# Kernel tuning notes

Hardware: AMD Instinct MI355X
Metric: run time of the kernel (lower is better)

Reference implementation:

```python
import jax, jax.numpy as jnp
import numpy as np

DIM = 512; H = 8; TEMP_LEN = 16; TARGET_LEN = 22
NT = TEMP_LEN ** 2          # 256 temp tokens
NS = TARGET_LEN ** 2        # 484 target tokens
N = NT + NS                 # 740
HD = DIM // H
SCALE = HD ** -0.5
EPS = 1e-5
B = 16


def _bias_index(L):
    coords = np.stack(np.meshgrid(np.arange(L), np.arange(L), indexing='ij')).reshape(2, -1)
    rel = (coords[:, :, None] - coords[:, None, :]).transpose(1, 2, 0)  # [L^2, L^2, 2]
    rel[..., 0] += L - 1
    rel[..., 1] += L - 1
    rel[..., 0] *= 2 * L - 1
    return jnp.asarray(rel.sum(-1))  # [L^2, L^2] indices into (2L-1)^2 table

TEMP_IDX = _bias_index(TEMP_LEN)
TARGET_IDX = _bias_index(TARGET_LEN)


def setup_inputs() -> dict:
    key = jax.random.key(0)
    ctr = iter(range(100))
    def nrm(shape, s=1.0):
        return jax.random.normal(jax.random.fold_in(key, next(ctr)), shape, jnp.float32) * s
    def uni(shape):
        return jax.random.uniform(jax.random.fold_in(key, next(ctr)), shape, jnp.float32, 0.5, 1.5)
    d = {'x': nrm((B, N, DIM))}
    for nm in ('q', 'k', 'v'):
        d[f'conv_{nm}_w'] = nrm((DIM, 1, 3, 3), 0.2)   # depthwise 3x3, groups=DIM
        d[f'bn_{nm}_g'] = 1.0 + nrm((DIM,), 0.1)
        d[f'bn_{nm}_b'] = nrm((DIM,), 0.1)
        d[f'bn_{nm}_m'] = nrm((DIM,), 0.1)
        d[f'bn_{nm}_v'] = uni((DIM,))
    for nm in ('q', 'k', 'v', 'p'):
        d[f'w{nm}'] = nrm((DIM, DIM), DIM ** -0.5)
        d[f'b{nm}'] = nrm((DIM,), 0.01)
    d['rpb_target'] = nrm(((2 * TARGET_LEN - 1) ** 2, H), 0.0002)
    d['rpb_temp'] = nrm(((2 * TEMP_LEN - 1) ** 2, 1), 0.0002)
    d['tt_bias'] = nrm((H, 1, NT), 0.0002)       # temp_target_bias_table
    d['tg_tm_bias'] = nrm((H, NS, 1), 0.0002)    # target_temp_bias_table
    return d


def _dwconv_bn(z, w, g, b, m, v):
    # z: [B, C, Hh, Ww]; depthwise conv + BatchNorm2d (inference stats)
    y = jax.lax.conv_general_dilated(z, w, (1, 1), ((1, 1), (1, 1)),
                                     dimension_numbers=('NCHW', 'OIHW', 'NCHW'),
                                     feature_group_count=DIM)
    inv = (g * jax.lax.rsqrt(v + EPS))[None, :, None, None]
    return (y - m[None, :, None, None]) * inv + b[None, :, None, None]


def reference(x, conv_q_w, bn_q_g, bn_q_b, bn_q_m, bn_q_v,
              conv_k_w, bn_k_g, bn_k_b, bn_k_m, bn_k_v,
              conv_v_w, bn_v_g, bn_v_b, bn_v_m, bn_v_v,
              wq, bq, wk, bk, wv, bv, wp, bp,
              rpb_target, rpb_temp, tt_bias, tg_tm_bias):
    Bb = x.shape[0]
    to_img = lambda t, L: t.transpose(0, 2, 1).reshape(Bb, DIM, L, L)
    to_seq = lambda t: t.reshape(Bb, DIM, -1).transpose(0, 2, 1)
    ti = to_img(x[:, :NT], TEMP_LEN)
    tg = to_img(x[:, NT:], TARGET_LEN)

    def conv_branch(w, g, b, m, v):
        return jnp.concatenate([to_seq(_dwconv_bn(ti, w, g, b, m, v)),
                                to_seq(_dwconv_bn(tg, w, g, b, m, v))], axis=1)

    q = conv_branch(conv_q_w, bn_q_g, bn_q_b, bn_q_m, bn_q_v) @ wq + bq
    k = conv_branch(conv_k_w, bn_k_g, bn_k_b, bn_k_m, bn_k_v) @ wk + bk
    v = conv_branch(conv_v_w, bn_v_g, bn_v_b, bn_v_m, bn_v_v) @ wv + bv

    heads = lambda t: t.reshape(Bb, -1, H, HD).transpose(0, 2, 1, 3)
    qtm, ktm, vtm = heads(q[:, :NT]), heads(k[:, :NT]), heads(v[:, :NT])
    qta, kh, vh = heads(q[:, NT:]), heads(k), heads(v)

    # gathered relative-position bias tables
    target_bias = rpb_target[TARGET_IDX.reshape(-1)].reshape(NS, NS, H).transpose(2, 0, 1)  # [H,NS,NS]
    temp_bias = rpb_temp[TEMP_IDX.reshape(-1)].reshape(NT, NT, 1).transpose(2, 0, 1)        # [1,NT,NT]
    padding = tt_bias + tg_tm_bias                                                          # [H,NS,NT]
    rel = jnp.concatenate([padding, target_bias], axis=2)                                   # [H,NS,N]

    # target -> all attention
    attn = jax.nn.softmax(jnp.einsum('bhqd,bhkd->bhqk', qta, kh) * SCALE + rel, axis=-1)
    out_t = jnp.einsum('bhqk,bhkd->bhqd', attn, vh).transpose(0, 2, 1, 3).reshape(Bb, NS, DIM)

    # temp -> temp attention (bias broadcast over heads)
    attn2 = jax.nn.softmax(jnp.einsum('bhqd,bhkd->bhqk', qtm, ktm) * SCALE + temp_bias, axis=-1)
    out_m = jnp.einsum('bhqk,bhkd->bhqd', attn2, vtm).transpose(0, 2, 1, 3).reshape(Bb, NT, DIM)

    return jnp.concatenate([out_m, out_t], axis=1) @ wp + bp
```

## Files before the change

kernel.cpp:

```cpp
#include <hip/hip_runtime.h>
#include <hip/hip_bf16.h>

typedef unsigned short u16;
typedef unsigned int u32;
typedef __attribute__((ext_vector_type(8))) short short8;
typedef __attribute__((ext_vector_type(4))) float f32x4;

#define NTOK 740
#define NTMP 256
#define NTGT 484
#define DM   512
#define MH   8
#define MROWS 11840
#define KPAD 768
#define LOG2E 1.4426950408889634f

__device__ __forceinline__ float b2f(u16 u) {
    union { unsigned int i; float f; } x; x.i = ((unsigned int)u) << 16; return x.f;
}
__device__ __forceinline__ u16 f2b(float f) {
    union { float f; unsigned int i; } x; x.f = f;
    unsigned int r = x.i + 0x7FFFu + ((x.i >> 16) & 1u);
    return (u16)(r >> 16);
}
__device__ __forceinline__ u32 pk2(float a, float b) {
    union { __hip_bfloat162 h; u32 u; } p;
    p.h = __float22bfloat162_rn(float2{a, b});
    return p.u;
}
__device__ __forceinline__ float fexp2(float x) {
    return __builtin_amdgcn_exp2f(x);
}
struct alignas(8) us4 { u16 x, y, z, w; };

__device__ __forceinline__ void gload16(const void* g, void* l) {
    __builtin_amdgcn_global_load_lds(
        (const __attribute__((address_space(1))) void*)g,
        (__attribute__((address_space(3))) void*)l, 16, 0, 0);
}

__global__ __launch_bounds__(256) void prep_all(
    const float* __restrict__ w0, const float* __restrict__ w1,
    const float* __restrict__ w2, const float* __restrict__ w3, u16* __restrict__ wTbase,
    const float* __restrict__ cw0, const float* __restrict__ g0, const float* __restrict__ bb0,
    const float* __restrict__ m0, const float* __restrict__ v0,
    const float* __restrict__ cw1, const float* __restrict__ g1, const float* __restrict__ bb1,
    const float* __restrict__ m1, const float* __restrict__ v1,
    const float* __restrict__ cw2, const float* __restrict__ g2, const float* __restrict__ bb2,
    const float* __restrict__ m2, const float* __restrict__ v2,
    float* __restrict__ cwfb, float* __restrict__ shb,
    const float* __restrict__ rpb_t, const float* __restrict__ tt,
    const float* __restrict__ tg, u16* __restrict__ btab,
    const float* __restrict__ rpb_m, u16* __restrict__ mtab) {
    __shared__ float t[32][33];
    const int id = blockIdx.x, tid = threadIdx.x;
    if (id < 1024) {
        const int z = id >> 8, rem = id & 255;
        const int bx = rem & 15, by = rem >> 4;
        const float* W = z == 0 ? w0 : z == 1 ? w1 : z == 2 ? w2 : w3;
        u16* WT = wTbase + (size_t)z * 262144;
        const int tx = tid & 31, ty = tid >> 5;
        for (int i = ty; i < 32; i += 8)
            t[i][tx] = W[(size_t)(by * 32 + i) * 512 + bx * 32 + tx];
        __syncthreads();
        for (int i = ty; i < 32; i += 8)
            WT[(size_t)(bx * 32 + i) * 512 + by * 32 + tx] = f2b(t[tx][i]);
    } else if (id < 1051) {
        const int rem = id - 1024;
        const int tap = rem % 9, br = rem / 9;
        const float* cw = br == 0 ? cw0 : br == 1 ? cw1 : cw2;
        const float* g  = br == 0 ? g0  : br == 1 ? g1  : g2;
        const float* bb = br == 0 ? bb0 : br == 1 ? bb1 : bb2;
        const float* m  = br == 0 ? m0  : br == 1 ? m1  : m2;
        const float* v  = br == 0 ? v0  : br == 1 ? v1  : v2;
        for (int c = tid; c < DM; c += 256) {
            const float inv = g[c] * rsqrtf(v[c] + 1e-5f);
            cwfb[(br * 9 + tap) * DM + c] = cw[c * 9 + tap] * inv;
            if (tap == 0) shb[br * DM + c] = bb[c] - m[c] * inv;
        }
    } else if (id < 4923) {
        const int rem = id - 1051;
        const int h = rem / NTGT, q = rem % NTGT;
        const int qh = q / 22, qw = q % 22;
        const float tgv = tg[h * NTGT + q];
        for (int k = tid; k < KPAD; k += 256) {
            float val;
            if (k < NTMP) val = (tt[h * NTMP + k] + tgv) * LOG2E;
            else if (k < NTOK) {
                const int kj = k - NTMP, kh = kj / 22, kw = kj % 22;
                val = rpb_t[((qh - kh + 21) * 43 + (qw - kw + 21)) * MH + h] * LOG2E;
            } else val = -1e30f;
            btab[((size_t)(h * NTGT + q)) * KPAD + k] = f2b(val);
        }
    } else {
        const int q = id - 4923, k = tid;
        const int qh = q >> 4, qw = q & 15, kh = k >> 4, kw = k & 15;
        mtab[q * 256 + k] = f2b(rpb_m[(qh - kh + 15) * 31 + (qw - kw + 15)] * LOG2E);
    }
}

__global__ __launch_bounds__(256) void conv_bn3(
    const float* __restrict__ x,
    const float* __restrict__ cwfb, const float* __restrict__ shb,
    u16* __restrict__ o0, u16* __restrict__ o1, u16* __restrict__ o2) {
    const int bn = blockIdx.x * 2 + (threadIdx.x >> 7);
    const int c = (threadIdx.x & 127) * 4;
    const int b = bn / NTOK, n = bn % NTOK;
    const bool tmp = n < NTMP;
    const int L = tmp ? 16 : 22, base = tmp ? 0 : NTMP, p = n - base;
    const int ph = p / L, pw = p % L;
    float4 xv[9];
#pragma unroll
    for (int tap = 0; tap < 9; ++tap) {
        const int dh = tap / 3 - 1, dw = tap % 3 - 1;
        const int h2 = ph + dh, w2 = pw + dw;
        const bool ok = (h2 >= 0 && h2 < L && w2 >= 0 && w2 < L);
        xv[tap] = ok ? *(const float4*)(x + (size_t)(b * NTOK + base + h2 * L + w2) * DM + c)
                     : float4{0.f, 0.f, 0.f, 0.f};
    }
    const size_t o = (size_t)bn * DM + c;
    u16* out[3] = {o0, o1, o2};
#pragma unroll
    for (int br = 0; br < 3; ++br) {
        float4 acc = *(const float4*)(shb + br * DM + c);
#pragma unroll
        for (int tap = 0; tap < 9; ++tap) {
            const float4 wv = *(const float4*)(cwfb + (br * 9 + tap) * DM + c);
            acc.x = fmaf(wv.x, xv[tap].x, acc.x);
            acc.y = fmaf(wv.y, xv[tap].y, acc.y);
            acc.z = fmaf(wv.z, xv[tap].z, acc.z);
            acc.w = fmaf(wv.w, xv[tap].w, acc.w);
        }
        us4 r;
        r.x = f2b(acc.x); r.y = f2b(acc.y); r.z = f2b(acc.z); r.w = f2b(acc.w);
        *(us4*)(out[br] + o) = r;
    }
}

#define GEMM_BODY(A, BT)                                                             \
    const int tid = threadIdx.x;                                                     \
    const int lane = tid & 63, w = tid >> 6;                                         \
    const int lr = lane & 15, lg = lane >> 4;                                        \
    const int wm = (w >> 1) * 32, wn = (w & 1) * 64;                                 \
    const int srow4 = lane >> 2;                                                     \
    const int sc = (lane & 3) ^ (srow4 & 3);                                         \
    const u16* asrc  = A  + (size_t)(gm0 + w * 16 + srow4) * 512 + sc * 8;           \
    const u16* bsrc0 = BT + (size_t)(gn0 + w * 32 + srow4) * 512 + sc * 8;           \
    const u16* bsrc1 = BT + (size_t)(gn0 + w * 32 + 16 + srow4) * 512 + sc * 8;      \
    f32x4 acc[2][4] = {};                                                            \
    gload16(asrc, &As[0][w * 512]);                                                  \
    gload16(bsrc0, &Bs[0][w * 1024]);                                                \
    gload16(bsrc1, &Bs[0][w * 1024 + 512]);                                          \
    for (int kt = 0; kt < 16; ++kt) {                                                \
        const int cur = kt & 1;                                                      \
        if (kt < 15) {                                                               \
            gload16(asrc + (kt + 1) * 32, &As[cur ^ 1][w * 512]);                    \
            gload16(bsrc0 + (kt + 1) * 32, &Bs[cur ^ 1][w * 1024]);                  \
            gload16(bsrc1 + (kt + 1) * 32, &Bs[cur ^ 1][w * 1024 + 512]);            \
            asm volatile("s_waitcnt vmcnt(3)" ::: "memory");                         \
        } else {                                                                     \
            asm volatile("s_waitcnt vmcnt(0)" ::: "memory");                         \
        }                                                                            \
        __syncthreads();                                                             \
        short8 af[2], bfr[4];                                                        \
        _Pragma("unroll")                                                            \
        for (int i = 0; i < 2; ++i)                                                  \
            af[i] = *(const short8*)&As[cur][(wm + i * 16 + lr) * 32 + (lg ^ (lr & 3)) * 8]; \
        _Pragma("unroll")                                                            \
        for (int j = 0; j < 4; ++j)                                                  \
            bfr[j] = *(const short8*)&Bs[cur][(wn + j * 16 + lr) * 32 + (lg ^ (lr & 3)) * 8]; \
        _Pragma("unroll")                                                            \
        for (int i = 0; i < 2; ++i)                                                  \
            _Pragma("unroll")                                                        \
            for (int j = 0; j < 4; ++j)                                              \
                acc[i][j] = __builtin_amdgcn_mfma_f32_16x16x32_bf16(af[i], bfr[j], acc[i][j], 0, 0, 0); \
        __syncthreads();                                                             \
    }

__device__ __forceinline__ int xcd_remap(int hw, int n) {
    const int q8 = n >> 3, r8 = n & 7;
    const int xcd = hw & 7, i8 = hw >> 3;
    return (xcd < r8 ? xcd * (q8 + 1) : r8 * (q8 + 1) + (xcd - r8) * q8) + i8;
}

__global__ __launch_bounds__(256) void gemm_qkv(
    const u16* __restrict__ Aq, const u16* __restrict__ Ak, const u16* __restrict__ Av,
    const u16* __restrict__ wTb, const float* __restrict__ bq,
    const float* __restrict__ bk, const float* __restrict__ bv,
    u16* __restrict__ qout, u16* __restrict__ kout, u16* __restrict__ vbT, int zbase) {
    __shared__ u16 As[2][2048];
    __shared__ u16 Bs[2][4096];
    const int hw = blockIdx.x + 185 * (blockIdx.y + 4 * blockIdx.z);
    const int lid = xcd_remap(hw, 740 * gridDim.z);
    const int by = lid & 3;
    const int bx = (lid >> 2) % 185;
    const int z = lid / 740 + zbase;
    const int gm0 = bx * 64, gn0 = by * 128;
    const u16* A = z == 0 ? Aq : z == 1 ? Ak : Av;
    const u16* BT = wTb + (size_t)z * 262144;
    const float* bias = z == 0 ? bq : z == 1 ? bk : bv;
    GEMM_BODY(A, BT)
    u16* lin = z == 0 ? qout : kout;
#pragma unroll
    for (int i = 0; i < 2; ++i)
#pragma unroll
        for (int j = 0; j < 4; ++j) {
            const int gc = gn0 + wn + j * 16 + lr;
            const float bvl = bias[gc];
#pragma unroll
            for (int r = 0; r < 4; ++r) {
                const int gr = gm0 + wm + i * 16 + lg * 4 + r;
                const float val = acc[i][j][r] + bvl;
                if (z == 2) {
                    const int b2 = gr / NTOK, k = gr - b2 * NTOK;
                    const int hh = gc >> 6, d = gc & 63;
                    vbT[((size_t)(b2 * MH + hh) * 64 + d) * KPAD + k] = f2b(val);
                } else {
                    lin[(size_t)gr * 512 + gc] = f2b(val);
                }
            }
        }
}

__global__ __launch_bounds__(256) void gemm_out(const u16* __restrict__ Ain,
                                                const u16* __restrict__ BTin,
                                                const float* __restrict__ bias,
                                                float* __restrict__ C) {
    __shared__ u16 As[2][2048];
    __shared__ u16 Bs[2][4096];
    const int hw = blockIdx.x + 185 * blockIdx.y;
    const int lid = xcd_remap(hw, 740);
    const int by = lid & 3;
    const int bx = lid >> 2;
    const int gm0 = bx * 64, gn0 = by * 128;
    GEMM_BODY(Ain, BTin)
#pragma unroll
    for (int i = 0; i < 2; ++i)
#pragma unroll
        for (int j = 0; j < 4; ++j) {
            const int gc = gn0 + wn + j * 16 + lr;
            const float bvl = bias[gc];
#pragma unroll
            for (int r = 0; r < 4; ++r) {
                const int gr = gm0 + wm + i * 16 + lg * 4 + r;
                C[(size_t)gr * 512 + gc] = acc[i][j][r] + bvl;
            }
        }
}

__global__ __launch_bounds__(256) void attn_all(const u16* __restrict__ qb,
                                                const u16* __restrict__ kb,
                                                const u16* __restrict__ vbT,
                                                const u16* __restrict__ btab,
                                                const u16* __restrict__ mtab,
                                                u16* __restrict__ attb) {
    __shared__ u16 Ks[2][32][64];
    __shared__ u16 VTs[2][64][32];
    __shared__ u16 Pb[2][4][16][32];

    int wg = blockIdx.x + 6 * (blockIdx.y + 8 * blockIdx.z);
    wg = (wg & 7) * 96 + (wg >> 3);
    const int bx = wg % 6;
    const int hb = wg / 6;
    const int h = hb & 7, b = hb >> 3;

    const bool tgt = bx < 4;
    const int q0 = (tgt ? bx : bx - 4) * 128;
    const int NKr = tgt ? NTOK : NTMP;
    const int NCH = tgt ? 24 : 8;
    const int QTOT = tgt ? NTGT : NTMP;
    const int QOFF = tgt ? NTMP : 0;
    const int TK = tgt ? KPAD : 256;
    const int tid = threadIdx.x;
    const int w = tid >> 6, lane = tid & 63;
    const int lq = lane & 15, lg = lane >> 4;
    const int fq = (lq & 3) ^ ((lq >> 2) & 3);
    const size_t brow = (size_t)b * NTOK;
    const float SCL = 0.125f * LOG2E;

    int qA = q0 + w * 16 + lq;       if (qA > QTOT - 1) qA = QTOT - 1;
    int qB = q0 + 64 + w * 16 + lq;  if (qB > QTOT - 1) qB = QTOT - 1;
    const u16* tbase = tgt ? (btab + (size_t)h * NTGT * KPAD) : mtab;
    const u16* trowA = tbase + (size_t)qA * TK;
    const u16* trowB = tbase + (size_t)qB * TK;

    short8 qfA[2], qfB[2];
#pragma unroll
    for (int dc = 0; dc < 2; ++dc) {
        qfA[dc] = *(const short8*)(qb + (brow + QOFF + qA) * DM + h * 64 + dc * 32 + lg * 8);
        qfB[dc] = *(const short8*)(qb + (brow + QOFF + qB) * DM + h * 64 + dc * 32 + lg * 8);
    }

    const int krow = tid >> 3, ksc = tid & 7;
    const int vrow = tid >> 2, vsc = tid & 3;
    const int fv = (vrow & 3) ^ ((vrow >> 2) & 3);
    const size_t vbase = (size_t)(b * MH + h) * 64 * KPAD;
    const u16* kptr2 = kb + brow * DM + h * 64 + (ksc ^ (krow & 7)) * 8;
    const u16* vptr2 = vbT + vbase + (size_t)vrow * KPAD + (vsc ^ fv) * 8;
    const int NKm1 = NKr - 1;

    float mrunA = -1e30f, lrunA = 0.f, mrunB = -1e30f, lrunB = 0.f;
    f32x4 oTA[4] = {}, oTB[4] = {};

    {
        const int keyc = krow < NKm1 ? krow : NKm1;
        gload16(kptr2 + (size_t)keyc * DM, &Ks[0][w * 8][0]);
        gload16(vptr2, &VTs[0][w * 16][0]);
    }
    us4 bcA0 = *(const us4*)(trowA + lg * 4);
    us4 bcA1 = *(const us4*)(trowA + 16 + lg * 4);
    us4 bcB0 = *(const us4*)(trowB + lg * 4);
    us4 bcB1 = *(const us4*)(trowB + 16 + lg * 4);
    asm volatile("s_waitcnt vmcnt(0)" ::: "memory");
    __syncthreads();

    for (int kc = 0; kc < NCH; ++kc) {
        const int cur = kc & 1, nxt = cur ^ 1;
        const bool more = (kc + 1 < NCH);
        us4 bnA0 = {0,0,0,0}, bnA1 = {0,0,0,0}, bnB0 = {0,0,0,0}, bnB1 = {0,0,0,0};
        if (more) {
            const int key = (kc + 1) * 32 + krow;
            const int keyc = key < NKm1 ? key : NKm1;
            gload16(kptr2 + (size_t)keyc * DM, &Ks[nxt][w * 8][0]);
            gload16(vptr2 + (kc + 1) * 32, &VTs[nxt][w * 16][0]);
            bnA0 = *(const us4*)(trowA + (kc + 1) * 32 + lg * 4);
            bnA1 = *(const us4*)(trowA + (kc + 1) * 32 + 16 + lg * 4);
            bnB0 = *(const us4*)(trowB + (kc + 1) * 32 + lg * 4);
            bnB1 = *(const us4*)(trowB + (kc + 1) * 32 + 16 + lg * 4);
        }

        f32x4 sA0 = {}, sA1 = {}, sB0 = {}, sB1 = {};
        __builtin_amdgcn_s_setprio(1);
#pragma unroll
        for (int dc = 0; dc < 2; ++dc) {
            short8 a0 = *(const short8*)&Ks[cur][lq][((dc * 4 + lg) ^ (lq & 7)) * 8];
            short8 a1 = *(const short8*)&Ks[cur][16 + lq][((dc * 4 + lg) ^ (lq & 7)) * 8];
            sA0 = __builtin_amdgcn_mfma_f32_16x16x32_bf16(a0, qfA[dc], sA0, 0, 0, 0);
            sB0 = __builtin_amdgcn_mfma_f32_16x16x32_bf16(a0, qfB[dc], sB0, 0, 0, 0);
            sA1 = __builtin_amdgcn_mfma_f32_16x16x32_bf16(a1, qfA[dc], sA1, 0, 0, 0);
            sB1 = __builtin_amdgcn_mfma_f32_16x16x32_bf16(a1, qfB[dc], sB1, 0, 0, 0);
        }
        __builtin_amdgcn_s_setprio(0);

        {
            float sv[8];
            sv[0] = fmaf(sA0[0], SCL, b2f(bcA0.x)); sv[1] = fmaf(sA0[1], SCL, b2f(bcA0.y));
            sv[2] = fmaf(sA0[2], SCL, b2f(bcA0.z)); sv[3] = fmaf(sA0[3], SCL, b2f(bcA0.w));
            sv[4] = fmaf(sA1[0], SCL, b2f(bcA1.x)); sv[5] = fmaf(sA1[1], SCL, b2f(bcA1.y));
            sv[6] = fmaf(sA1[2], SCL, b2f(bcA1.z)); sv[7] = fmaf(sA1[3], SCL, b2f(bcA1.w));
            float cm = sv[0];
#pragma unroll
            for (int i = 1; i < 8; ++i) cm = fmaxf(cm, sv[i]);
            cm = fmaxf(cm, __shfl_xor(cm, 16));
            cm = fmaxf(cm, __shfl_xor(cm, 32));
            if (!__all(cm <= mrunA)) {
                const float mnew = fmaxf(mrunA, cm);
                const float alpha = fexp2(mrunA - mnew);
#pragma unroll
                for (int t = 0; t < 4; ++t)
#pragma unroll
                    for (int r = 0; r < 4; ++r) oTA[t][r] *= alpha;
                lrunA *= alpha;
                mrunA = mnew;
            }
            float pv[8], psum = 0.f;
#pragma unroll
            for (int i = 0; i < 8; ++i) { pv[i] = fexp2(sv[i] - mrunA); psum += pv[i]; }
            const int c0 = (((lg >> 1) ^ fq) & 3) * 8 + (lg & 1) * 4;
            const int c1 = (((2 + (lg >> 1)) ^ fq) & 3) * 8 + (lg & 1) * 4;
            *(uint2*)&Pb[0][w][lq][c0] = uint2{pk2(pv[0], pv[1]), pk2(pv[2], pv[3])};
            *(uint2*)&Pb[0][w][lq][c1] = uint2{pk2(pv[4], pv[5]), pk2(pv[6], pv[7])};
            psum += __shfl_xor(psum, 16);
            psum += __shfl_xor(psum, 32);
            lrunA += psum;
        }
        {
            float sv[8];
            sv[0] = fmaf(sB0[0], SCL, b2f(bcB0.x)); sv[1] = fmaf(sB0[1], SCL, b2f(bcB0.y));
            sv[2] = fmaf(sB0[2], SCL, b2f(bcB0.z)); sv[3] = fmaf(sB0[3], SCL, b2f(bcB0.w));
            sv[4] = fmaf(sB1[0], SCL, b2f(bcB1.x)); sv[5] = fmaf(sB1[1], SCL, b2f(bcB1.y));
            sv[6] = fmaf(sB1[2], SCL, b2f(bcB1.z)); sv[7] = fmaf(sB1[3], SCL, b2f(bcB1.w));
            float cm = sv[0];
#pragma unroll
            for (int i = 1; i < 8; ++i) cm = fmaxf(cm, sv[i]);
            cm = fmaxf(cm, __shfl_xor(cm, 16));
            cm = fmaxf(cm, __shfl_xor(cm, 32));
            if (!__all(cm <= mrunB)) {
                const float mnew = fmaxf(mrunB, cm);
                const float alpha = fexp2(mrunB - mnew);
#pragma unroll
                for (int t = 0; t < 4; ++t)
#pragma unroll
                    for (int r = 0; r < 4; ++r) oTB[t][r] *= alpha;
                lrunB *= alpha;
                mrunB = mnew;
            }
            float pv[8], psum = 0.f;
#pragma unroll
            for (int i = 0; i < 8; ++i) { pv[i] = fexp2(sv[i] - mrunB); psum += pv[i]; }
            const int c0 = (((lg >> 1) ^ fq) & 3) * 8 + (lg & 1) * 4;
            const int c1 = (((2 + (lg >> 1)) ^ fq) & 3) * 8 + (lg & 1) * 4;
            *(uint2*)&Pb[1][w][lq][c0] = uint2{pk2(pv[0], pv[1]), pk2(pv[2], pv[3])};
            *(uint2*)&Pb[1][w][lq][c1] = uint2{pk2(pv[4], pv[5]), pk2(pv[6], pv[7])};
            psum += __shfl_xor(psum, 16);
            psum += __shfl_xor(psum, 32);
            lrunB += psum;
        }

        asm volatile("s_waitcnt lgkmcnt(0)" ::: "memory");

        short8 pfA = *(const short8*)&Pb[0][w][lq][((lg ^ fq) & 3) * 8];
        short8 pfB = *(const short8*)&Pb[1][w][lq][((lg ^ fq) & 3) * 8];
        __builtin_amdgcn_s_setprio(1);
#pragma unroll
        for (int t = 0; t < 4; ++t) {
            short8 vf = *(const short8*)&VTs[cur][t * 16 + lq][((lg ^ fq) & 3) * 8];
            oTA[t] = __builtin_amdgcn_mfma_f32_16x16x32_bf16(vf, pfA, oTA[t], 0, 0, 0);
            oTB[t] = __builtin_amdgcn_mfma_f32_16x16x32_bf16(vf, pfB, oTB[t], 0, 0, 0);
        }
        __builtin_amdgcn_s_setprio(0);

        bcA0 = bnA0; bcA1 = bnA1; bcB0 = bnB0; bcB1 = bnB1;
        asm volatile("s_waitcnt vmcnt(0)" ::: "memory");
        __syncthreads();
    }

    {
        const float linv = 1.f / lrunA;
        const int qrow = q0 + w * 16 + lq;
        if (qrow < QTOT) {
            u16* op = attb + (brow + QOFF + qrow) * DM + h * 64;
#pragma unroll
            for (int t = 0; t < 4; ++t)
                *(uint2*)(op + t * 16 + lg * 4) =
                    uint2{pk2(oTA[t][0] * linv, oTA[t][1] * linv),
                          pk2(oTA[t][2] * linv, oTA[t][3] * linv)};
        }
    }
    {
        const float linv = 1.f / lrunB;
        const int qrow = q0 + 64 + w * 16 + lq;
        if (qrow < QTOT) {
            u16* op = attb + (brow + QOFF + qrow) * DM + h * 64;
#pragma unroll
            for (int t = 0; t < 4; ++t)
                *(uint2*)(op + t * 16 + lg * 4) =
                    uint2{pk2(oTB[t][0] * linv, oTB[t][1] * linv),
                          pk2(oTB[t][2] * linv, oTB[t][3] * linv)};
        }
    }
}

extern "C" void kernel_launch(void* const* d_in, const int* in_sizes, int n_in,
                              void* d_out, int out_size, void* d_ws, size_t ws_size,
                              hipStream_t stream) {
    const float* x = (const float*)d_in[0];
    const float* convw[3] = {(const float*)d_in[1], (const float*)d_in[6], (const float*)d_in[11]};
    const float* bng[3]   = {(const float*)d_in[2], (const float*)d_in[7], (const float*)d_in[12]};
    const float* bnb[3]   = {(const float*)d_in[3], (const float*)d_in[8], (const float*)d_in[13]};
    const float* bnm[3]   = {(const float*)d_in[4], (const float*)d_in[9], (const float*)d_in[14]};
    const float* bnv[3]   = {(const float*)d_in[5], (const float*)d_in[10], (const float*)d_in[15]};
    const float* w[4]     = {(const float*)d_in[16], (const float*)d_in[18], (const float*)d_in[20], (const float*)d_in[22]};
    const float* bias[4]  = {(const float*)d_in[17], (const float*)d_in[19], (const float*)d_in[21], (const float*)d_in[23]};
    const float* rpb_t = (const float*)d_in[24];
    const float* rpb_m = (const float*)d_in[25];
    const float* tt    = (const float*)d_in[26];
    const float* tg    = (const float*)d_in[27];

    char* p = (char*)d_ws;
    auto alloc = [&](size_t n) { char* r = p; p += (n + 255) & ~(size_t)255; return r; };
    const size_t SEQ = (size_t)MROWS * DM * 2;
    u16* wTb  = (u16*)alloc(4 * 524288);
    u16* cbq  = (u16*)alloc(SEQ);
    u16* cbk  = (u16*)alloc(SEQ);
    u16* cbv  = (u16*)alloc(SEQ);
    u16* kbuf = (u16*)alloc(SEQ);
    u16* vbT  = (u16*)alloc((size_t)16 * MH * 64 * KPAD * 2);
    u16* btab = (u16*)alloc((size_t)MH * NTGT * KPAD * 2);
    u16* mtab = (u16*)alloc(256 * 256 * 2);
    float* cwf = (float*)alloc(3 * 9 * DM * 4);
    float* shf = (float*)alloc(3 * DM * 4);
    const size_t used = (size_t)(p - (char*)d_ws);
    const bool merged = ws_size >= used + SEQ;
    u16* qbuf = merged ? (u16*)alloc(SEQ) : cbv;
    u16* attb = cbq;

    prep_all<<<5179, 256, 0, stream>>>(
        w[0], w[1], w[2], w[3], wTb,
        convw[0], bng[0], bnb[0], bnm[0], bnv[0],
        convw[1], bng[1], bnb[1], bnm[1], bnv[1],
        convw[2], bng[2], bnb[2], bnm[2], bnv[2], cwf, shf,
        rpb_t, tt, tg, btab, rpb_m, mtab);

    conv_bn3<<<MROWS / 2, 256, 0, stream>>>(x, cwf, shf, cbq, cbk, cbv);

    if (merged) {
        gemm_qkv<<<dim3(185, 4, 3), 256, 0, stream>>>(cbq, cbk, cbv, wTb,
                                                      bias[0], bias[1], bias[2],
                                                      qbuf, kbuf, vbT, 0);
    } else {
        gemm_qkv<<<dim3(185, 4, 1), 256, 0, stream>>>(cbq, cbk, cbv, wTb,
                                                      bias[0], bias[1], bias[2],
                                                      qbuf, kbuf, vbT, 2);
        gemm_qkv<<<dim3(185, 4, 2), 256, 0, stream>>>(cbq, cbk, cbv, wTb,
                                                      bias[0], bias[1], bias[2],
                                                      qbuf, kbuf, vbT, 0);
    }

    attn_all<<<dim3(6, 8, 16), 256, 0, stream>>>(qbuf, kbuf, vbT, btab, mtab, attb);

    gemm_out<<<dim3(185, 4), 256, 0, stream>>>(attb, wTb + 3 * 262144, bias[3], (float*)d_out);
}
```

Before: 178.7 us.

## Triple-buffer GEMM LDS pipeline, widen swizzle, drop XCD block remap

```diff
diff --git a/kernel.cpp b/kernel.cpp
--- a/kernel.cpp
+++ b/kernel.cpp
@@ -137,65 +137,63 @@
     }
 }
 
+#define STAGE(bf, kk) do {                                                           \
+    gload16(asrc + (kk) * 32, &As[bf][w * 512]);                                     \
+    gload16(bsrc0 + (kk) * 32, &Bs[bf][w * 1024]);                                   \
+    gload16(bsrc1 + (kk) * 32, &Bs[bf][w * 1024 + 512]);                             \
+} while (0)
+
 #define GEMM_BODY(A, BT)                                                             \
     const int tid = threadIdx.x;                                                     \
     const int lane = tid & 63, w = tid >> 6;                                         \
     const int lr = lane & 15, lg = lane >> 4;                                        \
     const int wm = (w >> 1) * 32, wn = (w & 1) * 64;                                 \
     const int srow4 = lane >> 2;                                                     \
-    const int sc = (lane & 3) ^ (srow4 & 3);                                         \
+    const int sc = (lane & 3) ^ ((srow4 & 3) ^ ((srow4 >> 2) & 3));                  \
+    const int flr = (lr & 3) ^ ((lr >> 2) & 3);                                      \
     const u16* asrc  = A  + (size_t)(gm0 + w * 16 + srow4) * 512 + sc * 8;           \
     const u16* bsrc0 = BT + (size_t)(gn0 + w * 32 + srow4) * 512 + sc * 8;           \
     const u16* bsrc1 = BT + (size_t)(gn0 + w * 32 + 16 + srow4) * 512 + sc * 8;      \
     f32x4 acc[2][4] = {};                                                            \
-    gload16(asrc, &As[0][w * 512]);                                                  \
-    gload16(bsrc0, &Bs[0][w * 1024]);                                                \
-    gload16(bsrc1, &Bs[0][w * 1024 + 512]);                                          \
+    STAGE(0, 0); STAGE(1, 1);                                                        \
+    _Pragma("unroll")                                                                \
     for (int kt = 0; kt < 16; ++kt) {                                                \
-        const int cur = kt & 1;                                                      \
-        if (kt < 15) {                                                               \
-            gload16(asrc + (kt + 1) * 32, &As[cur ^ 1][w * 512]);                    \
-            gload16(bsrc0 + (kt + 1) * 32, &Bs[cur ^ 1][w * 1024]);                  \
-            gload16(bsrc1 + (kt + 1) * 32, &Bs[cur ^ 1][w * 1024 + 512]);            \
+        const int cur = kt % 3;                                                      \
+        if (kt < 14) {                                                               \
+            STAGE((kt + 2) % 3, kt + 2);                                             \
+            asm volatile("s_waitcnt vmcnt(6)" ::: "memory");                         \
+        } else if (kt == 14) {                                                       \
             asm volatile("s_waitcnt vmcnt(3)" ::: "memory");                         \
         } else {                                                                     \
             asm volatile("s_waitcnt vmcnt(0)" ::: "memory");                         \
         }                                                                            \
-        __syncthreads();                                                             \
+        __builtin_amdgcn_s_barrier();                                                \
+        asm volatile("" ::: "memory");                                               \
         short8 af[2], bfr[4];                                                        \
         _Pragma("unroll")                                                            \
         for (int i = 0; i < 2; ++i)                                                  \
-            af[i] = *(const short8*)&As[cur][(wm + i * 16 + lr) * 32 + (lg ^ (lr & 3)) * 8]; \
+            af[i] = *(const short8*)&As[cur][(wm + i * 16 + lr) * 32 + (lg ^ flr) * 8]; \
         _Pragma("unroll")                                                            \
         for (int j = 0; j < 4; ++j)                                                  \
-            bfr[j] = *(const short8*)&Bs[cur][(wn + j * 16 + lr) * 32 + (lg ^ (lr & 3)) * 8]; \
+            bfr[j] = *(const short8*)&Bs[cur][(wn + j * 16 + lr) * 32 + (lg ^ flr) * 8]; \
         _Pragma("unroll")                                                            \
         for (int i = 0; i < 2; ++i)                                                  \
             _Pragma("unroll")                                                        \
             for (int j = 0; j < 4; ++j)                                              \
                 acc[i][j] = __builtin_amdgcn_mfma_f32_16x16x32_bf16(af[i], bfr[j], acc[i][j], 0, 0, 0); \
-        __syncthreads();                                                             \
-    }
-
-__device__ __forceinline__ int xcd_remap(int hw, int n) {
-    const int q8 = n >> 3, r8 = n & 7;
-    const int xcd = hw & 7, i8 = hw >> 3;
-    return (xcd < r8 ? xcd * (q8 + 1) : r8 * (q8 + 1) + (xcd - r8) * q8) + i8;
-}
+        asm volatile("" ::: "memory");                                               \
+        __builtin_amdgcn_s_barrier();                                                \
+    }
 
 __global__ __launch_bounds__(256) void gemm_qkv(
     const u16* __restrict__ Aq, const u16* __restrict__ Ak, const u16* __restrict__ Av,
     const u16* __restrict__ wTb, const float* __restrict__ bq,
     const float* __restrict__ bk, const float* __restrict__ bv,
     u16* __restrict__ qout, u16* __restrict__ kout, u16* __restrict__ vbT, int zbase) {
-    __shared__ u16 As[2][2048];
-    __shared__ u16 Bs[2][4096];
-    const int hw = blockIdx.x + 185 * (blockIdx.y + 4 * blockIdx.z);
-    const int lid = xcd_remap(hw, 740 * gridDim.z);
-    const int by = lid & 3;
-    const int bx = (lid >> 2) % 185;
-    const int z = lid / 740 + zbase;
-    const int gm0 = bx * 64, gn0 = by * 128;
+    __shared__ u16 As[3][2048];
+    __shared__ u16 Bs[3][4096];
+    const int gm0 = blockIdx.x * 64, gn0 = blockIdx.y * 128;
+    const int z = blockIdx.z + zbase;
     const u16* A = z == 0 ? Aq : z == 1 ? Ak : Av;
     const u16* BT = wTb + (size_t)z * 262144;
     const float* bias = z == 0 ? bq : z == 1 ? bk : bv;
@@ -226,13 +224,9 @@
                                                 const u16* __restrict__ BTin,
                                                 const float* __restrict__ bias,
                                                 float* __restrict__ C) {
-    __shared__ u16 As[2][2048];
-    __shared__ u16 Bs[2][4096];
-    const int hw = blockIdx.x + 185 * blockIdx.y;
-    const int lid = xcd_remap(hw, 740);
-    const int by = lid & 3;
-    const int bx = lid >> 2;
-    const int gm0 = bx * 64, gn0 = by * 128;
+    __shared__ u16 As[3][2048];
+    __shared__ u16 Bs[3][4096];
+    const int gm0 = blockIdx.x * 64, gn0 = blockIdx.y * 128;
     GEMM_BODY(Ain, BTin)
 #pragma unroll
     for (int i = 0; i < 2; ++i)
```

After: 172.6 us. -3.4%, faster.
